# Performance work log

Hardware: AMD Instinct MI355X
Metric: run time of the kernel (lower is better)

Reference implementation:

```python
import jax, jax.numpy as jnp
import numpy as np
import math

K = 3
IN_CH = 512
OUT_CH = 512
W_DIM = 512
B = 16
HW = 64
LR_MUL = 1.0


def setup_inputs() -> dict:
    key = jax.random.key(0)
    k1, k2, k3, k4 = jax.random.split(key, 4)
    x = jax.random.normal(k1, (B, HW, HW, IN_CH), dtype=jnp.float32)
    w_latents = jax.random.normal(k2, (B, W_DIM), dtype=jnp.float32)
    w = jax.random.normal(k3, (K, K, IN_CH, OUT_CH), dtype=jnp.float32)  # init_std = 1/lr_mul = 1
    b = jnp.zeros((OUT_CH,), dtype=jnp.float32)
    fc_w = jax.random.normal(k4, (W_DIM, IN_CH), dtype=jnp.float32)
    fc_b = jnp.zeros((IN_CH,), dtype=jnp.float32)
    return {"x": x, "w_latents": w_latents, "w": w, "b": b, "fc_w": fc_w, "fc_b": fc_b}


def reference(x, w_latents, w, b, fc_w, fc_b):
    # equalized-LR runtime coefficients (gain=1)
    conv_coef = LR_MUL / math.sqrt(K * K * IN_CH)
    fc_coef = LR_MUL / math.sqrt(W_DIM)

    batch, H, W_, Cin = x.shape
    x_nchw = jnp.transpose(x, (0, 3, 1, 2))  # [B, Cin, H, W]

    weight = w * conv_coef  # [k,k,in,out]
    # style modulation: fully_connected (no lrelu) + 1
    s = w_latents @ (fc_w * fc_coef) + fc_b * LR_MUL + 1.0  # [B, in]

    # per-sample modulated weights [B,k,k,in,out]
    ww = weight[None] * s[:, None, None, :, None]
    # demodulation
    d = jax.lax.rsqrt(jnp.sum(jnp.square(ww), axis=(1, 2, 3)) + 1e-8)  # [B, out]
    ww = ww * d[:, None, None, None, :]

    # fused_modconv: grouped conv with groups = batch
    x_g = x_nchw.reshape(1, batch * Cin, H, W_)
    w_g = jnp.transpose(ww, (1, 2, 3, 0, 4)).reshape(K, K, Cin, batch * OUT_CH)
    y = jax.lax.conv_general_dilated(
        x_g, w_g,
        window_strides=(1, 1),
        padding='SAME',
        dimension_numbers=('NCHW', 'HWIO', 'NCHW'),
        feature_group_count=batch,
    )  # [1, B*out, H, W]
    y = y.reshape(batch, OUT_CH, H, W_)
    y = jnp.transpose(y, (0, 2, 3, 1))  # NHWC
    y = y + (b * LR_MUL)
    return y
```

## Files before the change

kernel.cpp:

```cpp
#include <hip/hip_runtime.h>
#include <hip/hip_bf16.h>

#define IN_CH 512
#define OUT_CH 512
#define W_DIM 512
#define BATCH 16
#define HWDIM 64
#define PADW 66

static constexpr float CONV_COEF = 0.014731391274719739f;
static constexpr float FC_COEF   = 0.044194173824159216f;

typedef __bf16 bf16x8 __attribute__((ext_vector_type(8)));
typedef float  f32x4  __attribute__((ext_vector_type(4)));

typedef __attribute__((address_space(1))) void gvoid;
typedef __attribute__((address_space(3))) void lvoid;

__device__ __forceinline__ void async_cp16(const void* g, void* l) {
    __builtin_amdgcn_global_load_lds((gvoid*)g, (lvoid*)l, 16, 0, 0);
}

__device__ __forceinline__ ushort f2bf(float f) {
    union { float f; unsigned u; } un; un.f = f;
    unsigned u = un.u;
    return (ushort)((u + 0x7fffu + ((u >> 16) & 1u)) >> 16);
}

__global__ void k_style(const float* __restrict__ wl, const float* __restrict__ fcw,
                        const float* __restrict__ fcb, float* __restrict__ s) {
    int b = blockIdx.x;
    int i = threadIdx.x;
    __shared__ float lw[W_DIM];
    lw[i] = wl[b * W_DIM + i];
    __syncthreads();
    float acc = 0.f;
#pragma unroll 8
    for (int j = 0; j < W_DIM; ++j) acc += lw[j] * fcw[(size_t)j * IN_CH + i];
    s[b * IN_CH + i] = acc * FC_COEF + fcb[i] + 1.0f;
}

__global__ void k_xs(const float* __restrict__ x, const float* __restrict__ s,
                     ushort* __restrict__ xs) {
    int t = blockIdx.x * blockDim.x + threadIdx.x;
    int pix = t >> 7;
    int c = (t & 127) << 2;
    int b = pix >> 12;
    int hw = pix & 4095;
    int h = hw >> 6, w = hw & 63;
    float4 xv = ((const float4*)x)[t];
    float4 sv = ((const float4*)(s + b * IN_CH))[t & 127];
    ushort4 o;
    o.x = f2bf(xv.x * sv.x);
    o.y = f2bf(xv.y * sv.y);
    o.z = f2bf(xv.z * sv.z);
    o.w = f2bf(xv.w * sv.w);
    size_t dst = (((size_t)(b * PADW + h + 1)) * PADW + (w + 1)) * IN_CH + c;
    *(ushort4*)(xs + dst) = o;
}

__global__ void k_wt(const float* __restrict__ w, ushort* __restrict__ wT) {
    __shared__ float tile[32][33];
    int kk = blockIdx.z;
    const float* src = w + (size_t)kk * IN_CH * OUT_CH;
    ushort* dst = wT + (size_t)kk * IN_CH * OUT_CH;
    int i0 = blockIdx.y * 32;
    int o0 = blockIdx.x * 32;
    int tx = threadIdx.x, ty = threadIdx.y;
#pragma unroll
    for (int rr = 0; rr < 32; rr += 8)
        tile[ty + rr][tx] = src[(size_t)(i0 + ty + rr) * OUT_CH + o0 + tx];
    __syncthreads();
#pragma unroll
    for (int rr = 0; rr < 32; rr += 8)
        dst[(size_t)(o0 + ty + rr) * IN_CH + i0 + tx] = f2bf(tile[tx][ty + rr]);
}

__global__ void k_a2(const float* __restrict__ w, float* __restrict__ a2) {
    int n = blockIdx.x * blockDim.x + threadIdx.x;
    float sum = 0.f;
#pragma unroll
    for (int kk = 0; kk < 9; ++kk) {
        float v = w[(size_t)kk * (IN_CH * OUT_CH) + n];
        sum += v * v;
    }
    a2[n] = sum;
}

__global__ void k_dmod(const float* __restrict__ s, const float* __restrict__ a2,
                       float* __restrict__ dmod) {
    int b = blockIdx.x, o = threadIdx.x;
    __shared__ float s2[IN_CH];
    float sv = s[b * IN_CH + o];
    s2[o] = sv * sv;
    __syncthreads();
    float acc = 0.f;
#pragma unroll 8
    for (int i = 0; i < IN_CH; ++i) acc += s2[i] * a2[(size_t)i * OUT_CH + o];
    dmod[b * OUT_CH + o] = rsqrtf(acc * CONV_COEF * CONV_COEF + 1e-8f);
}

__global__ __launch_bounds__(256) void k_conv(
    const ushort* __restrict__ xs, const ushort* __restrict__ wT,
    const float* __restrict__ dmod, const float* __restrict__ bias,
    float* __restrict__ out) {
    __shared__ ushort sA[128 * 32];
    __shared__ ushort sB[128 * 32];

    const int tid = threadIdx.x;
    const int wave = tid >> 6;
    const int lane = tid & 63;

    const int bid = blockIdx.x;
    const int nt = bid & 3;
    const int mt = bid >> 2;
    const int b  = mt >> 5;
    const int h0 = (mt & 31) << 1;
    const int n0 = nt << 7;

    const int mi = tid >> 2;
    const int p  = tid & 3;
    const int k8 = p ^ ((mi >> 1) & 3);

    const ushort* gA0 = xs + (((size_t)(b * PADW + h0)) * PADW + mi) * IN_CH + k8 * 8;
    const ushort* gA1 = gA0 + (size_t)PADW * IN_CH;
    const ushort* gB0 = wT + ((size_t)(n0 + mi)) * IN_CH + k8 * 8;
    const ushort* gB1 = gB0 + (size_t)64 * IN_CH;

    ushort* dA0 = sA + wave * 512;
    ushort* dA1 = sA + 2048 + wave * 512;
    ushort* dB0 = sB + wave * 512;
    ushort* dB1 = sB + 2048 + wave * 512;

    const int r = lane & 15;
    const int q = lane >> 4;
    const int pq = q ^ ((r >> 1) & 3);
    const int wr = (wave & 1) << 6;
    const int wc = (wave >> 1) << 6;

    const ushort* aRd[4];
    const ushort* bRd[4];
#pragma unroll
    for (int f = 0; f < 4; ++f) {
        aRd[f] = sA + (wr + f * 16 + r) * 32 + pq * 8;
        bRd[f] = sB + (wc + f * 16 + r) * 32 + pq * 8;
    }

    f32x4 acc[4][4];
#pragma unroll
    for (int i = 0; i < 4; ++i)
#pragma unroll
        for (int j = 0; j < 4; ++j) {
            f32x4 z = {0.f, 0.f, 0.f, 0.f};
            acc[i][j] = z;
        }

    for (int kk = 0; kk < 9; ++kk) {
        const int aoff = ((kk / 3) * PADW + (kk % 3)) * IN_CH;
        const int boff = kk * (IN_CH * OUT_CH);
        for (int c0 = 0; c0 < IN_CH; c0 += 32) {
            __syncthreads();
            async_cp16(gA0 + aoff + c0, dA0);
            async_cp16(gA1 + aoff + c0, dA1);
            async_cp16(gB0 + boff + c0, dB0);
            async_cp16(gB1 + boff + c0, dB1);
            __syncthreads();
            bf16x8 av[4], bv[4];
#pragma unroll
            for (int f = 0; f < 4; ++f) av[f] = *(const bf16x8*)aRd[f];
#pragma unroll
            for (int f = 0; f < 4; ++f) bv[f] = *(const bf16x8*)bRd[f];
#pragma unroll
            for (int i = 0; i < 4; ++i)
#pragma unroll
                for (int j = 0; j < 4; ++j)
                    acc[i][j] = __builtin_amdgcn_mfma_f32_16x16x32_bf16(
                        av[i], bv[j], acc[i][j], 0, 0, 0);
        }
    }

#pragma unroll
    for (int j = 0; j < 4; ++j) {
        const int n = n0 + wc + j * 16 + r;
        const float scale = dmod[b * OUT_CH + n] * CONV_COEF;
        const float bv2 = bias[n];
#pragma unroll
        for (int i = 0; i < 4; ++i) {
#pragma unroll
            for (int e = 0; e < 4; ++e) {
                const int m = wr + i * 16 + q * 4 + e;
                const int h = h0 + (m >> 6);
                const int w = m & 63;
                out[(((size_t)(b * HWDIM + h)) * HWDIM + w) * OUT_CH + n] =
                    acc[i][j][e] * scale + bv2;
            }
        }
    }
}

extern "C" void kernel_launch(void* const* d_in, const int* in_sizes, int n_in,
                              void* d_out, int out_size, void* d_ws, size_t ws_size,
                              hipStream_t stream) {
    const float* x    = (const float*)d_in[0];
    const float* wl   = (const float*)d_in[1];
    const float* w    = (const float*)d_in[2];
    const float* bias = (const float*)d_in[3];
    const float* fcw  = (const float*)d_in[4];
    const float* fcb  = (const float*)d_in[5];
    float* out = (float*)d_out;

    char* ws = (char*)d_ws;
    const size_t XS_BYTES = (size_t)BATCH * PADW * PADW * IN_CH * 2;
    const size_t WT_BYTES = (size_t)9 * IN_CH * OUT_CH * 2;
    ushort* xs   = (ushort*)ws;
    ushort* wT   = (ushort*)(ws + XS_BYTES);
    float*  s    = (float*)(ws + XS_BYTES + WT_BYTES);
    float*  dmod = s + BATCH * IN_CH;
    float*  a2   = dmod + BATCH * OUT_CH;

    hipMemsetAsync(xs, 0, XS_BYTES, stream);
    k_style<<<BATCH, W_DIM, 0, stream>>>(wl, fcw, fcb, s);
    k_xs<<<(BATCH * HWDIM * HWDIM * IN_CH / 4) / 256, 256, 0, stream>>>(x, s, xs);
    k_wt<<<dim3(16, 16, 9), dim3(32, 8), 0, stream>>>(w, wT);
    k_a2<<<(IN_CH * OUT_CH) / 256, 256, 0, stream>>>(w, a2);
    k_dmod<<<BATCH, OUT_CH, 0, stream>>>(s, a2, dmod);
    k_conv<<<2048, 256, 0, stream>>>(xs, wT, dmod, bias, out);
}
```

Before: 675.1 us.

## Double conv K-chunk to 64 with XOR swizzle, zero only halo, remap block order

The conv kernel now stages 64 input channels per LDS iteration instead of 32, using an 8-way XOR swizzle. This halves the number of barrier pairs per tile, and the block index is remapped so neighbouring blocks share A tiles across the N tiles for better L2 reuse. The full memset of the padded activation buffer is replaced by a small kernel that zeroes only the halo border, which removes a large write pass. The style and demod kernels are split over more blocks for parallelism. LDS use doubles to 32KB per block, which may lower occupancy.

```diff
diff --git a/kernel.cpp b/kernel.cpp
--- a/kernel.cpp
+++ b/kernel.cpp
@@ -27,12 +27,26 @@
     return (ushort)((u + 0x7fffu + ((u >> 16) & 1u)) >> 16);
 }
 
+__global__ void k_halo(ushort* __restrict__ xs) {
+    int b = blockIdx.y;
+    int pidx = blockIdx.x * 4 + (threadIdx.x >> 6);
+    int ch = threadIdx.x & 63;
+    int h, w;
+    if (pidx < 66)       { h = 0;          w = pidx; }
+    else if (pidx < 132) { h = 65;         w = pidx - 66; }
+    else if (pidx < 196) { h = pidx - 131; w = 0; }
+    else                 { h = pidx - 195; w = 65; }
+    size_t base = (((size_t)(b * PADW + h)) * PADW + w) * IN_CH + ch * 8;
+    uint4 z = {0u, 0u, 0u, 0u};
+    *(uint4*)(xs + base) = z;
+}
+
 __global__ void k_style(const float* __restrict__ wl, const float* __restrict__ fcw,
                         const float* __restrict__ fcb, float* __restrict__ s) {
     int b = blockIdx.x;
-    int i = threadIdx.x;
+    int i = blockIdx.y * 128 + threadIdx.x;
     __shared__ float lw[W_DIM];
-    lw[i] = wl[b * W_DIM + i];
+    for (int j = threadIdx.x; j < W_DIM; j += 128) lw[j] = wl[b * W_DIM + j];
     __syncthreads();
     float acc = 0.f;
 #pragma unroll 8
@@ -89,10 +103,13 @@
 
 __global__ void k_dmod(const float* __restrict__ s, const float* __restrict__ a2,
                        float* __restrict__ dmod) {
-    int b = blockIdx.x, o = threadIdx.x;
+    int b = blockIdx.x;
+    int o = blockIdx.y * 128 + threadIdx.x;
     __shared__ float s2[IN_CH];
-    float sv = s[b * IN_CH + o];
-    s2[o] = sv * sv;
+    for (int i = threadIdx.x; i < IN_CH; i += 128) {
+        float v = s[b * IN_CH + i];
+        s2[i] = v * v;
+    }
     __syncthreads();
     float acc = 0.f;
 #pragma unroll 8
@@ -104,47 +121,57 @@
     const ushort* __restrict__ xs, const ushort* __restrict__ wT,
     const float* __restrict__ dmod, const float* __restrict__ bias,
     float* __restrict__ out) {
-    __shared__ ushort sA[128 * 32];
-    __shared__ ushort sB[128 * 32];
+    __shared__ ushort sA[128 * 64];
+    __shared__ ushort sB[128 * 64];
 
     const int tid = threadIdx.x;
     const int wave = tid >> 6;
     const int lane = tid & 63;
 
     const int bid = blockIdx.x;
-    const int nt = bid & 3;
-    const int mt = bid >> 2;
+    const int mt = (bid & 7) | ((bid >> 5) << 3);
+    const int nt = (bid >> 3) & 3;
     const int b  = mt >> 5;
     const int h0 = (mt & 31) << 1;
     const int n0 = nt << 7;
 
-    const int mi = tid >> 2;
-    const int p  = tid & 3;
-    const int k8 = p ^ ((mi >> 1) & 3);
-
-    const ushort* gA0 = xs + (((size_t)(b * PADW + h0)) * PADW + mi) * IN_CH + k8 * 8;
-    const ushort* gA1 = gA0 + (size_t)PADW * IN_CH;
-    const ushort* gB0 = wT + ((size_t)(n0 + mi)) * IN_CH + k8 * 8;
-    const ushort* gB1 = gB0 + (size_t)64 * IN_CH;
-
-    ushort* dA0 = sA + wave * 512;
-    ushort* dA1 = sA + 2048 + wave * 512;
-    ushort* dB0 = sB + wave * 512;
-    ushort* dB1 = sB + 2048 + wave * 512;
+    const int srow = tid >> 3;
+    const int lc   = (tid & 7) ^ (srow & 7);
+
+    const ushort* gA[4];
+    const ushort* gB[4];
+#pragma unroll
+    for (int i = 0; i < 4; ++i) {
+        int row = i * 32 + srow;
+        int rh  = row >> 6;
+        int w   = row & 63;
+        gA[i] = xs + (((size_t)(b * PADW + h0 + rh)) * PADW + w) * IN_CH + lc * 8;
+        gB[i] = wT + ((size_t)(n0 + row)) * IN_CH + lc * 8;
+    }
+    ushort* dA[4];
+    ushort* dB[4];
+#pragma unroll
+    for (int i = 0; i < 4; ++i) {
+        dA[i] = sA + (i * 256 + wave * 64) * 8;
+        dB[i] = sB + (i * 256 + wave * 64) * 8;
+    }
 
     const int r = lane & 15;
     const int q = lane >> 4;
-    const int pq = q ^ ((r >> 1) & 3);
     const int wr = (wave & 1) << 6;
     const int wc = (wave >> 1) << 6;
 
-    const ushort* aRd[4];
-    const ushort* bRd[4];
-#pragma unroll
-    for (int f = 0; f < 4; ++f) {
-        aRd[f] = sA + (wr + f * 16 + r) * 32 + pq * 8;
-        bRd[f] = sB + (wc + f * 16 + r) * 32 + pq * 8;
-    }
+    const ushort* aRd[2][4];
+    const ushort* bRd[2][4];
+#pragma unroll
+    for (int ks = 0; ks < 2; ++ks)
+#pragma unroll
+        for (int f = 0; f < 4; ++f) {
+            int rowA = wr + f * 16 + r;
+            aRd[ks][f] = sA + rowA * 64 + ((ks * 4 + q) ^ (rowA & 7)) * 8;
+            int rowB = wc + f * 16 + r;
+            bRd[ks][f] = sB + rowB * 64 + ((ks * 4 + q) ^ (rowB & 7)) * 8;
+        }
 
     f32x4 acc[4][4];
 #pragma unroll
@@ -157,25 +184,29 @@
 
     for (int kk = 0; kk < 9; ++kk) {
         const int aoff = ((kk / 3) * PADW + (kk % 3)) * IN_CH;
-        const int boff = kk * (IN_CH * OUT_CH);
-        for (int c0 = 0; c0 < IN_CH; c0 += 32) {
+        const size_t boff = (size_t)kk * (IN_CH * OUT_CH);
+        for (int c0 = 0; c0 < IN_CH; c0 += 64) {
             __syncthreads();
-            async_cp16(gA0 + aoff + c0, dA0);
-            async_cp16(gA1 + aoff + c0, dA1);
-            async_cp16(gB0 + boff + c0, dB0);
-            async_cp16(gB1 + boff + c0, dB1);
+#pragma unroll
+            for (int i = 0; i < 4; ++i) {
+                async_cp16(gA[i] + aoff + c0, dA[i]);
+                async_cp16(gB[i] + boff + c0, dB[i]);
+            }
             __syncthreads();
-            bf16x8 av[4], bv[4];
-#pragma unroll
-            for (int f = 0; f < 4; ++f) av[f] = *(const bf16x8*)aRd[f];
-#pragma unroll
-            for (int f = 0; f < 4; ++f) bv[f] = *(const bf16x8*)bRd[f];
-#pragma unroll
-            for (int i = 0; i < 4; ++i)
-#pragma unroll
-                for (int j = 0; j < 4; ++j)
-                    acc[i][j] = __builtin_amdgcn_mfma_f32_16x16x32_bf16(
-                        av[i], bv[j], acc[i][j], 0, 0, 0);
+#pragma unroll
+            for (int ks = 0; ks < 2; ++ks) {
+                bf16x8 av[4], bv[4];
+#pragma unroll
+                for (int f = 0; f < 4; ++f) av[f] = *(const bf16x8*)aRd[ks][f];
+#pragma unroll
+                for (int f = 0; f < 4; ++f) bv[f] = *(const bf16x8*)bRd[ks][f];
+#pragma unroll
+                for (int i = 0; i < 4; ++i)
+#pragma unroll
+                    for (int j = 0; j < 4; ++j)
+                        acc[i][j] = __builtin_amdgcn_mfma_f32_16x16x32_bf16(
+                            av[i], bv[j], acc[i][j], 0, 0, 0);
+            }
         }
     }
 
@@ -218,11 +249,11 @@
     float*  dmod = s + BATCH * IN_CH;
     float*  a2   = dmod + BATCH * OUT_CH;
 
-    hipMemsetAsync(xs, 0, XS_BYTES, stream);
-    k_style<<<BATCH, W_DIM, 0, stream>>>(wl, fcw, fcb, s);
+    k_halo<<<dim3(65, BATCH), 256, 0, stream>>>(xs);
+    k_style<<<dim3(BATCH, 4), 128, 0, stream>>>(wl, fcw, fcb, s);
     k_xs<<<(BATCH * HWDIM * HWDIM * IN_CH / 4) / 256, 256, 0, stream>>>(x, s, xs);
     k_wt<<<dim3(16, 16, 9), dim3(32, 8), 0, stream>>>(w, wT);
     k_a2<<<(IN_CH * OUT_CH) / 256, 256, 0, stream>>>(w, a2);
-    k_dmod<<<BATCH, OUT_CH, 0, stream>>>(s, a2, dmod);
+    k_dmod<<<dim3(BATCH, 4), 128, 0, stream>>>(s, a2, dmod);
     k_conv<<<2048, 256, 0, stream>>>(xs, wT, dmod, bias, out);
 }
```

Measured after the change: 571.4 us. 15.4% less time.
